# Optimization experiments

Measured on AMD Instinct MI355X. Metric: run time of the kernel, lower is better.

Reference implementation:

```python
import jax, jax.numpy as jnp
import numpy as np

SOBEL = np.array([[1, 0, -1], [2, 0, -2], [1, 0, -1]], dtype=np.float32)


def _conv3(x, w):
    # 3x3 conv, stride 1, padding 1, no bias (NCHW / OIHW)
    return jax.lax.conv_general_dilated(
        x, w, window_strides=(1, 1), padding='SAME',
        dimension_numbers=('NCHW', 'OIHW', 'NCHW'))


def _sobel_conv(x, wx, wy, w1, b1):
    # |sobel_x| + |sobel_y| followed by 1x1 conv (w1: [O, C])
    e = jnp.abs(_conv3(x, wx)) + jnp.abs(_conv3(x, wy))
    return jnp.einsum('bchw,oc->bohw', e, w1) + b1[None, :, None, None]


def setup_inputs() -> dict:
    key = jax.random.key(0)
    ks = jax.random.split(key, 12)
    B, C, H, W = 2, 64, 64, 64
    dk = C // 8
    sob = jnp.asarray(SOBEL)
    inp = {
        'vi': jax.random.normal(ks[0], (B, C, H, W), jnp.float32),
        'ir': jax.random.normal(ks[1], (B, C, H, W), jnp.float32),
        # Sobel conv weights: torch copy_ broadcasts the 3x3 kernel over [C,C,3,3]
        'wsx_vi': jnp.broadcast_to(sob, (C, C, 3, 3)).copy(),
        'wsy_vi': jnp.broadcast_to(sob.T, (C, C, 3, 3)).copy(),
        'w1_vi': jax.random.normal(ks[2], (dk, C), jnp.float32) * 0.05,
        'b1_vi': jax.random.normal(ks[3], (dk,), jnp.float32) * 0.05,
        'wsx_q': jnp.broadcast_to(sob, (2 * C, 2 * C, 3, 3)).copy(),
        'wsy_q': jnp.broadcast_to(sob.T, (2 * C, 2 * C, 3, 3)).copy(),
        'w1_q': jax.random.normal(ks[4], (dk, 2 * C), jnp.float32) * 0.05,
        'b1_q': jax.random.normal(ks[5], (dk,), jnp.float32) * 0.05,
        'wsx_ir': jnp.broadcast_to(sob, (C, C, 3, 3)).copy(),
        'wsy_ir': jnp.broadcast_to(sob.T, (C, C, 3, 3)).copy(),
        'w1_ir': jax.random.normal(ks[6], (dk, C), jnp.float32) * 0.05,
        'b1_ir': jax.random.normal(ks[7], (dk,), jnp.float32) * 0.05,
        'wv_vi': jax.random.normal(ks[8], (C, C), jnp.float32) * 0.05,
        'bv_vi': jax.random.normal(ks[9], (C,), jnp.float32) * 0.05,
        'wv_ir': jax.random.normal(ks[10], (C, C), jnp.float32) * 0.05,
        'bv_ir': jax.random.normal(ks[11], (C,), jnp.float32) * 0.05,
    }
    return inp


def reference(vi, ir, wsx_vi, wsy_vi, w1_vi, b1_vi, wsx_q, wsy_q, w1_q, b1_q,
              wsx_ir, wsy_ir, w1_ir, b1_ir, wv_vi, bv_vi, wv_ir, bv_ir):
    B, C, H, W = vi.shape
    N = H * W
    # Query from concatenated modalities: [B, N, dk]
    xq = _sobel_conv(jnp.concatenate([vi, ir], axis=1), wsx_q, wsy_q, w1_q, b1_q)
    xq = xq.reshape(B, -1, N).transpose(0, 2, 1)
    # Keys: [B, dk, N]
    vi_xk = _sobel_conv(vi, wsx_vi, wsy_vi, w1_vi, b1_vi).reshape(B, -1, N)
    ir_xk = _sobel_conv(ir, wsx_ir, wsy_ir, w1_ir, b1_ir).reshape(B, -1, N)
    # Values (1x1 convs): [B, C, N]
    vi_xv = (jnp.einsum('bchw,oc->bohw', vi, wv_vi) + bv_vi[None, :, None, None]).reshape(B, C, N)
    ir_xv = (jnp.einsum('bchw,oc->bohw', ir, wv_ir) + bv_ir[None, :, None, None]).reshape(B, C, N)
    # Unscaled attention, softmax over last dim: [B, N, N]
    vi_attn = jax.nn.softmax(jnp.einsum('bnd,bdm->bnm', xq, vi_xk), axis=-1)
    ir_attn = jax.nn.softmax(jnp.einsum('bnd,bdm->bnm', xq, ir_xk), axis=-1)
    # Cross combination: vi value routed by ir attention (and vice versa)
    vi_out = jnp.einsum('bcn,bmn->bcm', vi_xv, ir_attn).reshape(B, C, H, W)
    ir_out = jnp.einsum('bcn,bmn->bcm', ir_xv, vi_attn).reshape(B, C, H, W)
    return vi_out, ir_out
```

## Files before the change

kernel.cpp:

```cpp
#include <hip/hip_runtime.h>
#include <hip/hip_bf16.h>

typedef __attribute__((ext_vector_type(8))) short bf16x8;
typedef __attribute__((ext_vector_type(8))) __bf16 bf16v8;
typedef __attribute__((ext_vector_type(4))) float f32x4;
typedef __attribute__((ext_vector_type(4))) int   i32x4;

#if __has_builtin(__builtin_amdgcn_exp2f)
#define EXP2(x) __builtin_amdgcn_exp2f(x)
#else
#define EXP2(x) exp2f(x)
#endif


__global__ __launch_bounds__(256) void kP_prep(
    const float* __restrict__ vi, const float* __restrict__ ir,
    const float* __restrict__ w1_vi, const float* __restrict__ w1_q,
    const float* __restrict__ b1_q,  const float* __restrict__ w1_ir,
    const float* __restrict__ wv_vi, const float* __restrict__ bv_vi,
    const float* __restrict__ wv_ir, const float* __restrict__ bv_ir,
    float* __restrict__ s, float* __restrict__ scal,
    __hip_bfloat16* __restrict__ Vc) {
    const int t = threadIdx.x;
    if (blockIdx.x < 256) {
        __shared__ __align__(16) char wlds[64 * 128];
        const int bm = blockIdx.x >> 6, nt = blockIdx.x & 63;
        const int b = bm >> 1, mod = bm & 1;
        const float* wv = mod ? wv_ir : wv_vi;
        const float* bv = mod ? bv_ir : bv_vi;
        const float* x = (mod ? ir : vi) + b * (64 * 4096);
        {
            const float* src = wv + t * 16;
            int row = t >> 2, colb = (t & 3) * 32;
            bf16v8 lo8, hi8;
            #pragma unroll
            for (int j = 0; j < 8; ++j) {
                lo8[j] = (__bf16)src[j];
                hi8[j] = (__bf16)src[8 + j];
            }
            int sw = (row & 7) << 4;
            *(i32x4*)(wlds + row * 128 + (colb ^ sw)) = __builtin_bit_cast(i32x4, lo8);
            *(i32x4*)(wlds + row * 128 + ((colb + 16) ^ sw)) = __builtin_bit_cast(i32x4, hi8);
        }
        __syncthreads();
        const int wvid = t >> 6, lane = t & 63;
        const int col = lane & 15, g = lane >> 4;
        const int n = nt * 64 + wvid * 16 + col;
        bf16x8 afr[4][2];
        #pragma unroll
        for (int cb = 0; cb < 4; ++cb) {
            int row = cb * 16 + col;
            int sw = (row & 7) << 4;
            #pragma unroll
            for (int ks = 0; ks < 2; ++ks)
                afr[cb][ks] = *(const bf16x8*)(wlds + row * 128 + ((ks * 64 + g * 16) ^ sw));
        }
        float ssum = 0.f;
        bf16x8 bfr[2];
        #pragma unroll
        for (int ks = 0; ks < 2; ++ks) {
            const float* xr = x + (ks * 32 + g * 8) * 4096 + n;
            bf16v8 pb;
            #pragma unroll
            for (int j = 0; j < 8; ++j) {
                float v = xr[j * 4096];
                ssum += v;
                pb[j] = (__bf16)v;
            }
            bfr[ks] = __builtin_bit_cast(bf16x8, pb);
        }
        ssum += __shfl_xor(ssum, 16);
        ssum += __shfl_xor(ssum, 32);
        if (lane < 16) s[bm * 4096 + nt * 64 + wvid * 16 + lane] = ssum;

        f32x4 acc[4];
        #pragma unroll
        for (int cb = 0; cb < 4; ++cb)
            #pragma unroll
            for (int r = 0; r < 4; ++r) acc[cb][r] = bv[cb * 16 + g * 4 + r];
        #pragma unroll
        for (int ks = 0; ks < 2; ++ks)
            #pragma unroll
            for (int cb = 0; cb < 4; ++cb)
                acc[cb] = __builtin_amdgcn_mfma_f32_16x16x32_bf16(afr[cb][ks], bfr[ks], acc[cb], 0, 0, 0);
        __hip_bfloat16* outp = Vc + (size_t)(bm * 64) * 4096 + n;
        #pragma unroll
        for (int cb = 0; cb < 4; ++cb)
            #pragma unroll
            for (int r = 0; r < 4; ++r)
                outp[(cb * 16 + g * 4 + r) * 4096] = __float2bfloat16(acc[cb][r]);
    } else {
        __shared__ float Ad[8], Cv[8], Ci[8], Bq[8];
        if (t < 8) {
            float a = 0.f;
            for (int c = 0; c < 128; ++c) a += w1_q[t * 128 + c];
            float cv = 0.f, ci = 0.f;
            for (int c = 0; c < 64; ++c) { cv += w1_vi[t * 64 + c]; ci += w1_ir[t * 64 + c]; }
            Ad[t] = a; Cv[t] = cv; Ci[t] = ci; Bq[t] = b1_q[t];
        }
        __syncthreads();
        if (t == 0) {
            float av = 0, gv = 0, ai = 0, gi = 0;
            for (int d = 0; d < 8; ++d) {
                av += Ad[d] * Cv[d]; gv += Bq[d] * Cv[d];
                ai += Ad[d] * Ci[d]; gi += Bq[d] * Ci[d];
            }
            scal[0] = av; scal[1] = gv; scal[2] = ai; scal[3] = gi;
        }
    }
}

#define CH 512
#define NCH 8
__global__ __launch_bounds__(512, 2) void k4_attn(
        const float* __restrict__ s, const float* __restrict__ scal,
        const float* __restrict__ wsx_vi, const float* __restrict__ wsy_vi,
        const float* __restrict__ wsx_q,  const float* __restrict__ wsy_q,
        const float* __restrict__ wsx_ir, const float* __restrict__ wsy_ir,
        const __hip_bfloat16* __restrict__ Vc, float* __restrict__ out) {
    __shared__ __align__(16) char smem[147456];
    __shared__ float mm[16];
    char* vbuf0 = smem;
    char* vbuf1 = smem + 65536;
    float* elds = (float*)(smem + 131072);
    const int mt = blockIdx.x;
    const int bw = blockIdx.y;
    const int b = bw >> 1, which = bw & 1;
    const int amod = which ? 0 : 1;
    const float* wsxa = amod ? wsx_ir : wsx_vi;
    const float* wsya = amod ? wsy_ir : wsy_vi;
    const float alpha = scal[which ? 0 : 2];
    const float gamma = scal[which ? 1 : 3];
    const short* Vg = (const short*)(Vc + (size_t)(bw * 64) * 4096);

    const int tid = threadIdx.x;
    const int wvw = tid >> 6, lane = tid & 63;
    const int col = lane & 15, g = lane >> 4;

    float* sld = (float*)vbuf0;
    const float* sg = s + (size_t)(b * 2) * 4096;
    #pragma unroll
    for (int k = 0; k < 16; ++k) { int i = tid + k * 512; sld[i] = sg[i]; }
    __syncthreads();

    float mn = 3.0e38f, mx = 0.f;
    {
        const float* sa = sld + amod * 4096;
        #pragma unroll
        for (int k2 = 0; k2 < 8; ++k2) {
            int n = tid + k2 * 512;
            int hh = n >> 6, ww = n & 63;
            float gx = 0.f, gy = 0.f;
            #pragma unroll
            for (int di = 0; di < 3; ++di)
                #pragma unroll
                for (int dj = 0; dj < 3; ++dj) {
                    int r = hh + di - 1, c2 = ww + dj - 1;
                    bool in = (r >= 0) & (r < 64) & (c2 >= 0) & (c2 < 64);
                    float v = in ? sa[r * 64 + c2] : 0.f;
                    int kk = di * 3 + dj;
                    gx = fmaf(v, wsxa[kk], gx);
                    gy = fmaf(v, wsya[kk], gy);
                }
            float ev = fabsf(gx) + fabsf(gy);
            elds[n] = ev;
            mn = fminf(mn, ev); mx = fmaxf(mx, ev);
        }
    }
    float eq[4];
    #pragma unroll
    for (int mg = 0; mg < 4; ++mg) {
        int ww = mg * 16 + col;
        float gx = 0.f, gy = 0.f;
        #pragma unroll
        for (int di = 0; di < 3; ++di)
            #pragma unroll
            for (int dj = 0; dj < 3; ++dj) {
                int r = mt + di - 1, c2 = ww + dj - 1;
                bool in = (r >= 0) & (r < 64) & (c2 >= 0) & (c2 < 64);
                float v = in ? (sld[r * 64 + c2] + sld[4096 + r * 64 + c2]) : 0.f;
                int kk = di * 3 + dj;
                gx = fmaf(v, wsx_q[kk], gx);
                gy = fmaf(v, wsy_q[kk], gy);
            }
        eq[mg] = fabsf(gx) + fabsf(gy);
    }
    #pragma unroll
    for (int o = 32; o; o >>= 1) {
        mn = fminf(mn, __shfl_xor(mn, o));
        mx = fmaxf(mx, __shfl_xor(mx, o));
    }
    if (lane == 0) { mm[wvw] = mn; mm[8 + wvw] = mx; }
    __syncthreads();
    float emn = mm[0], emx = mm[8];
    #pragma unroll
    for (int w = 1; w < 8; ++w) {
        emn = fminf(emn, mm[w]); emx = fmaxf(emx, mm[8 + w]);
    }
    const float L2E = 1.4426950408889634f;
    float t2[4], nM2[4];
    #pragma unroll
    for (int mg = 0; mg < 4; ++mg) {
        float t = alpha * eq[mg] + gamma;
        t2[mg]  = t * L2E;
        nM2[mg] = -((t > 0.f) ? t * emx : t * emn) * L2E;
    }

    #pragma unroll
    for (int k = 0; k < 8; ++k) {
        int id = tid + k * 512;
        int c = id >> 6, ss = id & 63;
        bf16x8 v = *(const bf16x8*)(Vg + c * 4096 + ss * 8);
        *(bf16x8*)(vbuf0 + c * 1024 + ((ss * 16) ^ ((c & 31) << 4))) = v;
    }
    __syncthreads();

    f32x4 acc[4][4] = {};
    f32x4 accz[4] = {};
    bf16x8 ones;
    #pragma unroll
    for (int j = 0; j < 8; ++j) ones[j] = (short)0x3F80;

    for (int ck = 0; ck < NCH; ++ck) {
        bf16x8 stg[8];
        const bool pf = (ck + 1 < NCH);
        if (pf) {
            const short* src = Vg + (ck + 1) * CH;
            #pragma unroll
            for (int k = 0; k < 8; ++k) {
                int id = tid + k * 512;
                int c = id >> 6, ss = id & 63;
                stg[k] = *(const bf16x8*)(src + c * 4096 + ss * 8);
            }
        }
        const char* vb = (ck & 1) ? vbuf1 : vbuf0;
        const float* el = elds + ck * CH;
        #pragma unroll
        for (int j = 0; j < 2; ++j) {
            const int n0 = (wvw * 2 + j) * 32;
            bf16x8 af[4];
            #pragma unroll
            for (int cb = 0; cb < 4; ++cb) {
                int row = cb * 16 + col;
                int byte = row * 1024 + (((n0 + g * 8) * 2) ^ ((row & 31) << 4));
                af[cb] = *(const bf16x8*)(vb + byte);
            }
            f32x4 e0 = *(const f32x4*)(el + n0 + g * 8);
            f32x4 e1 = *(const f32x4*)(el + n0 + g * 8 + 4);
            #pragma unroll
            for (int mg = 0; mg < 4; ++mg) {
                bf16v8 pb;
                #pragma unroll
                for (int q = 0; q < 4; ++q) {
                    float g0 = fmaf(e0[q], t2[mg], nM2[mg]);
                    float g1 = fmaf(e1[q], t2[mg], nM2[mg]);
                    pb[q]     = (__bf16)EXP2(g0);
                    pb[q + 4] = (__bf16)EXP2(g1);
                }
                bf16x8 bfrag = __builtin_bit_cast(bf16x8, pb);
                #pragma unroll
                for (int cb = 0; cb < 4; ++cb)
                    acc[mg][cb] = __builtin_amdgcn_mfma_f32_16x16x32_bf16(af[cb], bfrag, acc[mg][cb], 0, 0, 0);
                accz[mg] = __builtin_amdgcn_mfma_f32_16x16x32_bf16(ones, bfrag, accz[mg], 0, 0, 0);
            }
        }
        __syncthreads();
        if (pf) {
            char* wb = (ck & 1) ? vbuf0 : vbuf1;
            #pragma unroll
            for (int k = 0; k < 8; ++k) {
                int id = tid + k * 512;
                int c = id >> 6, ss = id & 63;
                *(bf16x8*)(wb + c * 1024 + ((ss * 16) ^ ((c & 31) << 4))) = stg[k];
            }
            __syncthreads();
        }
    }

    float* rbuf = (float*)smem;
    #pragma unroll
    for (int mg = 0; mg < 4; ++mg) {
        int base = ((wvw * 4 + mg) * 64 + lane) * 17;
        #pragma unroll
        for (int cb = 0; cb < 4; ++cb)
            *(f32x4*)(rbuf + base + cb * 4) = acc[mg][cb];
        rbuf[base + 16] = accz[mg][0];
    }
    __syncthreads();
    {
        const int mg = wvw & 3, hh = wvw >> 2;
        f32x4 sum0 = {}, sum1 = {};
        float z = 0.f;
        #pragma unroll
        for (int src = 0; src < 8; ++src) {
            int sb = ((src * 4 + mg) * 64 + lane) * 17;
            sum0 += *(const f32x4*)(rbuf + sb + (hh * 2 + 0) * 4);
            sum1 += *(const f32x4*)(rbuf + sb + (hh * 2 + 1) * 4);
            z += rbuf[sb + 16];
        }
        float inv = 1.0f / z;
        int m = mt * 64 + mg * 16 + col;
        float* ob = out + which * (2 * 64 * 4096) + b * (64 * 4096) + m;
        int c0 = (hh * 2) * 16 + g * 4;
        int c1 = (hh * 2 + 1) * 16 + g * 4;
        #pragma unroll
        for (int r = 0; r < 4; ++r) ob[(c0 + r) * 4096] = sum0[r] * inv;
        #pragma unroll
        for (int r = 0; r < 4; ++r) ob[(c1 + r) * 4096] = sum1[r] * inv;
    }
}

extern "C" void kernel_launch(void* const* d_in, const int* in_sizes, int n_in,
                              void* d_out, int out_size, void* d_ws, size_t ws_size,
                              hipStream_t stream) {
    const float* vi     = (const float*)d_in[0];
    const float* ir     = (const float*)d_in[1];
    const float* wsx_vi = (const float*)d_in[2];
    const float* wsy_vi = (const float*)d_in[3];
    const float* w1_vi  = (const float*)d_in[4];
    const float* wsx_q  = (const float*)d_in[6];
    const float* wsy_q  = (const float*)d_in[7];
    const float* w1_q   = (const float*)d_in[8];
    const float* b1_q   = (const float*)d_in[9];
    const float* wsx_ir = (const float*)d_in[10];
    const float* wsy_ir = (const float*)d_in[11];
    const float* w1_ir  = (const float*)d_in[12];
    const float* wv_vi  = (const float*)d_in[14];
    const float* bv_vi  = (const float*)d_in[15];
    const float* wv_ir  = (const float*)d_in[16];
    const float* bv_ir  = (const float*)d_in[17];
    (void)in_sizes; (void)n_in; (void)out_size;

    char* ws = (char*)d_ws;
    float* scal = (float*)ws;
    float* s    = (float*)(ws + 1280);
    __hip_bfloat16* Vc = (__hip_bfloat16*)(ws + 1280 + 65536);
    float* out = (float*)d_out;
    (void)ws_size;

    kP_prep<<<dim3(257), 256, 0, stream>>>(vi, ir, w1_vi, w1_q, b1_q, w1_ir,
                                           wv_vi, bv_vi, wv_ir, bv_ir, s, scal, Vc);
    k4_attn<<<dim3(64, 4), 512, 0, stream>>>(s, scal, wsx_vi, wsy_vi, wsx_q, wsy_q,
                                             wsx_ir, wsy_ir, Vc, out);
}
```

Baseline: 37.66 us.

## Double attention block to 1024 threads, splitting query tiles across waves

Moves the attention kernel from 512 to 1024 threads per block. Each of the 16 waves now owns one 16-query tile and a quarter of the key range within each chunk, instead of all four query tiles over an eighth of the chunk. This cuts per-thread accumulator registers and raises wave-level parallelism per CU. In exchange, the cross-wave reduction becomes a four-way split where one quarter of the waves do the final sum and the stores, and the exp work is now computed per query tile rather than shared.

New measurement: 32.41 us. 14.0% less time.

```diff
diff --git a/kernel.cpp b/kernel.cpp
--- a/kernel.cpp
+++ b/kernel.cpp
@@ -112,14 +112,14 @@
 
 #define CH 512
 #define NCH 8
-__global__ __launch_bounds__(512, 2) void k4_attn(
+__global__ __launch_bounds__(1024) void k4_attn(
         const float* __restrict__ s, const float* __restrict__ scal,
         const float* __restrict__ wsx_vi, const float* __restrict__ wsy_vi,
         const float* __restrict__ wsx_q,  const float* __restrict__ wsy_q,
         const float* __restrict__ wsx_ir, const float* __restrict__ wsy_ir,
         const __hip_bfloat16* __restrict__ Vc, float* __restrict__ out) {
     __shared__ __align__(16) char smem[147456];
-    __shared__ float mm[16];
+    __shared__ float mm[32];
     char* vbuf0 = smem;
     char* vbuf1 = smem + 65536;
     float* elds = (float*)(smem + 131072);
@@ -135,20 +135,21 @@
 
     const int tid = threadIdx.x;
     const int wvw = tid >> 6, lane = tid & 63;
+    const int h = wvw >> 2, wvt = wvw & 3;
     const int col = lane & 15, g = lane >> 4;
 
     float* sld = (float*)vbuf0;
     const float* sg = s + (size_t)(b * 2) * 4096;
     #pragma unroll
-    for (int k = 0; k < 16; ++k) { int i = tid + k * 512; sld[i] = sg[i]; }
+    for (int k = 0; k < 8; ++k) { int i = tid + k * 1024; sld[i] = sg[i]; }
     __syncthreads();
 
     float mn = 3.0e38f, mx = 0.f;
     {
         const float* sa = sld + amod * 4096;
         #pragma unroll
-        for (int k2 = 0; k2 < 8; ++k2) {
-            int n = tid + k2 * 512;
+        for (int k2 = 0; k2 < 4; ++k2) {
+            int n = tid + k2 * 1024;
             int hh = n >> 6, ww = n & 63;
             float gx = 0.f, gy = 0.f;
             #pragma unroll
@@ -167,10 +168,9 @@
             mn = fminf(mn, ev); mx = fmaxf(mx, ev);
         }
     }
-    float eq[4];
-    #pragma unroll
-    for (int mg = 0; mg < 4; ++mg) {
-        int ww = mg * 16 + col;
+    float eq;
+    {
+        int ww = wvt * 16 + col;
         float gx = 0.f, gy = 0.f;
         #pragma unroll
         for (int di = 0; di < 3; ++di)
@@ -183,52 +183,48 @@
                 gx = fmaf(v, wsx_q[kk], gx);
                 gy = fmaf(v, wsy_q[kk], gy);
             }
-        eq[mg] = fabsf(gx) + fabsf(gy);
+        eq = fabsf(gx) + fabsf(gy);
     }
     #pragma unroll
     for (int o = 32; o; o >>= 1) {
         mn = fminf(mn, __shfl_xor(mn, o));
         mx = fmaxf(mx, __shfl_xor(mx, o));
     }
-    if (lane == 0) { mm[wvw] = mn; mm[8 + wvw] = mx; }
+    if (lane == 0) { mm[wvw] = mn; mm[16 + wvw] = mx; }
     __syncthreads();
-    float emn = mm[0], emx = mm[8];
-    #pragma unroll
-    for (int w = 1; w < 8; ++w) {
-        emn = fminf(emn, mm[w]); emx = fmaxf(emx, mm[8 + w]);
+    float emn = mm[0], emx = mm[16];
+    #pragma unroll
+    for (int w = 1; w < 16; ++w) {
+        emn = fminf(emn, mm[w]); emx = fmaxf(emx, mm[16 + w]);
     }
     const float L2E = 1.4426950408889634f;
-    float t2[4], nM2[4];
-    #pragma unroll
-    for (int mg = 0; mg < 4; ++mg) {
-        float t = alpha * eq[mg] + gamma;
-        t2[mg]  = t * L2E;
-        nM2[mg] = -((t > 0.f) ? t * emx : t * emn) * L2E;
-    }
-
-    #pragma unroll
-    for (int k = 0; k < 8; ++k) {
-        int id = tid + k * 512;
+    const float t  = alpha * eq + gamma;
+    const float t2 = t * L2E;
+    const float nM2 = -((t > 0.f) ? t * emx : t * emn) * L2E;
+
+    #pragma unroll
+    for (int k = 0; k < 4; ++k) {
+        int id = tid + k * 1024;
         int c = id >> 6, ss = id & 63;
         bf16x8 v = *(const bf16x8*)(Vg + c * 4096 + ss * 8);
         *(bf16x8*)(vbuf0 + c * 1024 + ((ss * 16) ^ ((c & 31) << 4))) = v;
     }
     __syncthreads();
 
-    f32x4 acc[4][4] = {};
-    f32x4 accz[4] = {};
+    f32x4 acc[4] = {};
+    f32x4 accz = {};
     bf16x8 ones;
     #pragma unroll
     for (int j = 0; j < 8; ++j) ones[j] = (short)0x3F80;
 
     for (int ck = 0; ck < NCH; ++ck) {
-        bf16x8 stg[8];
+        bf16x8 stg[4];
         const bool pf = (ck + 1 < NCH);
         if (pf) {
             const short* src = Vg + (ck + 1) * CH;
             #pragma unroll
-            for (int k = 0; k < 8; ++k) {
-                int id = tid + k * 512;
+            for (int k = 0; k < 4; ++k) {
+                int id = tid + k * 1024;
                 int c = id >> 6, ss = id & 63;
                 stg[k] = *(const bf16x8*)(src + c * 4096 + ss * 8);
             }
@@ -236,8 +232,8 @@
         const char* vb = (ck & 1) ? vbuf1 : vbuf0;
         const float* el = elds + ck * CH;
         #pragma unroll
-        for (int j = 0; j < 2; ++j) {
-            const int n0 = (wvw * 2 + j) * 32;
+        for (int j = 0; j < 4; ++j) {
+            const int n0 = (h * 4 + j) * 32;
             bf16x8 af[4];
             #pragma unroll
             for (int cb = 0; cb < 4; ++cb) {
@@ -247,29 +243,26 @@
             }
             f32x4 e0 = *(const f32x4*)(el + n0 + g * 8);
             f32x4 e1 = *(const f32x4*)(el + n0 + g * 8 + 4);
-            #pragma unroll
-            for (int mg = 0; mg < 4; ++mg) {
-                bf16v8 pb;
-                #pragma unroll
-                for (int q = 0; q < 4; ++q) {
-                    float g0 = fmaf(e0[q], t2[mg], nM2[mg]);
-                    float g1 = fmaf(e1[q], t2[mg], nM2[mg]);
-                    pb[q]     = (__bf16)EXP2(g0);
-                    pb[q + 4] = (__bf16)EXP2(g1);
-                }
-                bf16x8 bfrag = __builtin_bit_cast(bf16x8, pb);
-                #pragma unroll
-                for (int cb = 0; cb < 4; ++cb)
-                    acc[mg][cb] = __builtin_amdgcn_mfma_f32_16x16x32_bf16(af[cb], bfrag, acc[mg][cb], 0, 0, 0);
-                accz[mg] = __builtin_amdgcn_mfma_f32_16x16x32_bf16(ones, bfrag, accz[mg], 0, 0, 0);
-            }
+            bf16v8 pb;
+            #pragma unroll
+            for (int q = 0; q < 4; ++q) {
+                float g0 = fmaf(e0[q], t2, nM2);
+                float g1 = fmaf(e1[q], t2, nM2);
+                pb[q]     = (__bf16)EXP2(g0);
+                pb[q + 4] = (__bf16)EXP2(g1);
+            }
+            bf16x8 bfrag = __builtin_bit_cast(bf16x8, pb);
+            #pragma unroll
+            for (int cb = 0; cb < 4; ++cb)
+                acc[cb] = __builtin_amdgcn_mfma_f32_16x16x32_bf16(af[cb], bfrag, acc[cb], 0, 0, 0);
+            accz = __builtin_amdgcn_mfma_f32_16x16x32_bf16(ones, bfrag, accz, 0, 0, 0);
         }
         __syncthreads();
         if (pf) {
             char* wb = (ck & 1) ? vbuf0 : vbuf1;
             #pragma unroll
-            for (int k = 0; k < 8; ++k) {
-                int id = tid + k * 512;
+            for (int k = 0; k < 4; ++k) {
+                int id = tid + k * 1024;
                 int c = id >> 6, ss = id & 63;
                 *(bf16x8*)(wb + c * 1024 + ((ss * 16) ^ ((c & 31) << 4))) = stg[k];
             }
@@ -277,36 +270,34 @@
         }
     }
 
-    float* rbuf = (float*)smem;
-    #pragma unroll
-    for (int mg = 0; mg < 4; ++mg) {
-        int base = ((wvw * 4 + mg) * 64 + lane) * 17;
+    float* rbuf = (float*)vbuf0;
+    if (h > 0) {
+        int base = (((h - 1) * 4 + wvt) * 64 + lane) * 17;
         #pragma unroll
         for (int cb = 0; cb < 4; ++cb)
-            *(f32x4*)(rbuf + base + cb * 4) = acc[mg][cb];
-        rbuf[base + 16] = accz[mg][0];
+            *(f32x4*)(rbuf + base + cb * 4) = acc[cb];
+        rbuf[base + 16] = accz[0];
     }
     __syncthreads();
-    {
-        const int mg = wvw & 3, hh = wvw >> 2;
-        f32x4 sum0 = {}, sum1 = {};
-        float z = 0.f;
-        #pragma unroll
-        for (int src = 0; src < 8; ++src) {
-            int sb = ((src * 4 + mg) * 64 + lane) * 17;
-            sum0 += *(const f32x4*)(rbuf + sb + (hh * 2 + 0) * 4);
-            sum1 += *(const f32x4*)(rbuf + sb + (hh * 2 + 1) * 4);
+    if (h == 0) {
+        float z = accz[0];
+        #pragma unroll
+        for (int src = 0; src < 3; ++src) {
+            int sb = ((src * 4 + wvt) * 64 + lane) * 17;
+            #pragma unroll
+            for (int cb = 0; cb < 4; ++cb)
+                acc[cb] += *(const f32x4*)(rbuf + sb + cb * 4);
             z += rbuf[sb + 16];
         }
         float inv = 1.0f / z;
-        int m = mt * 64 + mg * 16 + col;
+        int m = mt * 64 + wvt * 16 + col;
         float* ob = out + which * (2 * 64 * 4096) + b * (64 * 4096) + m;
-        int c0 = (hh * 2) * 16 + g * 4;
-        int c1 = (hh * 2 + 1) * 16 + g * 4;
-        #pragma unroll
-        for (int r = 0; r < 4; ++r) ob[(c0 + r) * 4096] = sum0[r] * inv;
-        #pragma unroll
-        for (int r = 0; r < 4; ++r) ob[(c1 + r) * 4096] = sum1[r] * inv;
+        #pragma unroll
+        for (int cb = 0; cb < 4; ++cb) {
+            int c = cb * 16 + g * 4;
+            #pragma unroll
+            for (int r = 0; r < 4; ++r) ob[(c + r) * 4096] = acc[cb][r] * inv;
+        }
     }
 }
 
@@ -340,6 +331,6 @@
 
     kP_prep<<<dim3(257), 256, 0, stream>>>(vi, ir, w1_vi, w1_q, b1_q, w1_ir,
                                            wv_vi, bv_vi, wv_ir, bv_ir, s, scal, Vc);
-    k4_attn<<<dim3(64, 4), 512, 0, stream>>>(s, scal, wsx_vi, wsy_vi, wsx_q, wsy_q,
-                                             wsx_ir, wsy_ir, Vc, out);
+    k4_attn<<<dim3(64, 4), 1024, 0, stream>>>(s, scal, wsx_vi, wsy_vi, wsx_q, wsy_q,
+                                              wsx_ir, wsy_ir, Vc, out);
 }
```
